# Performance work log

Hardware: AMD Instinct MI355X
Metric: run time of the kernel (lower is better)

## Reference

```python
import jax, jax.numpy as jnp
import numpy as np

B, T, I, Hd = 64, 1024, 256, 256
SIGMA = 0.01


def setup_inputs() -> dict:
    key = jax.random.key(0)
    ks = jax.random.split(key, 7)
    return {
        "inputs": jax.random.normal(ks[0], (B, T, I), dtype=jnp.float32),
        "W_xz": jax.random.normal(ks[1], (I, Hd), dtype=jnp.float32) * SIGMA,
        "W_hz": jax.random.normal(ks[2], (Hd, Hd), dtype=jnp.float32) * SIGMA,
        "b_z": jnp.zeros((Hd,), dtype=jnp.float32),
        "W_xr": jax.random.normal(ks[3], (I, Hd), dtype=jnp.float32) * SIGMA,
        "W_hr": jax.random.normal(ks[4], (Hd, Hd), dtype=jnp.float32) * SIGMA,
        "b_r": jnp.zeros((Hd,), dtype=jnp.float32),
        "W_xh": jax.random.normal(ks[5], (I, Hd), dtype=jnp.float32) * SIGMA,
        "W_hh": jax.random.normal(ks[6], (Hd, Hd), dtype=jnp.float32) * SIGMA,
        "b_h": jnp.zeros((Hd,), dtype=jnp.float32),
    }


def reference(inputs, W_xz, W_hz, b_z, W_xr, W_hr, b_r, W_xh, W_hh, b_h):
    # inputs: [B, T, I] -> time-major [T, B, I]
    xs = jnp.swapaxes(inputs, 0, 1)
    # Precompute all input-side projections in three big GEMMs (same math,
    # hoisted out of the recurrence): [T, B, Hd] each.
    xz = jnp.einsum("tbi,ih->tbh", xs, W_xz) + b_z
    xr = jnp.einsum("tbi,ih->tbh", xs, W_xr) + b_r
    xh = jnp.einsum("tbi,ih->tbh", xs, W_xh) + b_h

    H0 = jnp.zeros((inputs.shape[0], W_hz.shape[0]), dtype=inputs.dtype)

    def step(H, x):
        xz_t, xr_t, xh_t = x
        Z = jax.nn.sigmoid(xz_t + H @ W_hz)
        R = jax.nn.sigmoid(xr_t + H @ W_hr)
        H_tilde = jnp.tanh(xh_t + (R * H) @ W_hh)
        H_new = Z * H + (1.0 - Z) * H_tilde
        return H_new, H_new

    H_last, outs = jax.lax.scan(step, H0, (xz, xr, xh))
    # outputs stacked along dim=1: [B, T, Hd]
    outputs = jnp.swapaxes(outs, 0, 1)
    return outputs, H_last
```

## Files before the change

### kernel.cpp

```cpp
#include <hip/hip_runtime.h>
#include <math.h>

#define BB 64
#define TT 1024
#define II 256
#define HD 256

typedef unsigned short ushort_t;
typedef unsigned int uint_t;

typedef short sh8 __attribute__((ext_vector_type(8)));
typedef float fx4 __attribute__((ext_vector_type(4)));
typedef uint_t u32x4 __attribute__((ext_vector_type(4)));

__device__ __forceinline__ ushort_t f2bf(float f) {
    uint_t u = __float_as_uint(f);
    uint_t r = (u + 0x7fffu + ((u >> 16) & 1u)) >> 16;
    return (ushort_t)r;
}
__device__ __forceinline__ float bf2f(ushort_t v) {
    return __uint_as_float(((uint_t)v) << 16);
}

__device__ __forceinline__ float fast_rcp(float x) {
#if __has_builtin(__builtin_amdgcn_rcpf)
    return __builtin_amdgcn_rcpf(x);
#else
    return 1.f / x;
#endif
}
__device__ __forceinline__ float sigm(float x) {
    return fast_rcp(1.f + __expf(-x));
}
__device__ __forceinline__ float tanh_fast(float x) {
    return 1.f - 2.f * fast_rcp(1.f + __expf(2.f * x));
}

__device__ __forceinline__ fx4 mfma16(sh8 a, sh8 b, fx4 c) {
    return __builtin_amdgcn_mfma_f32_16x16x32_bf16(a, b, c, 0, 0, 0);
}

__device__ __forceinline__ void split2(float a, float b, uint_t& hi, uint_t& lo) {
    const uint_t ua = __float_as_uint(a), ub = __float_as_uint(b);
    hi = (ua >> 16) | (ub & 0xffff0000u);
    const float la = a - __uint_as_float(ua & 0xffff0000u);
    const float lb = b - __uint_as_float(ub & 0xffff0000u);
    const uint_t ula = __float_as_uint(la), ulb = __float_as_uint(lb);
    lo = (ula >> 16) | (ulb & 0xffff0000u);
}

__device__ __forceinline__ void async_g2l(const ushort_t* g, ushort_t* l) {
#if __has_builtin(__builtin_amdgcn_global_load_lds)
    __builtin_amdgcn_global_load_lds(
        (const __attribute__((address_space(1))) unsigned int*)g,
        (__attribute__((address_space(3))) unsigned int*)l, 16, 0, 0);
#else
    *reinterpret_cast<uint4*>(l) = *reinterpret_cast<const uint4*>(g);
#endif
}

#define BAR() asm volatile("s_waitcnt lgkmcnt(0)\n\ts_barrier" ::: "memory")

__global__ __launch_bounds__(256) void prepack_kernel(
    const float* __restrict__ Wz, const float* __restrict__ Wr,
    const float* __restrict__ Wh,
    const float* __restrict__ Xz, const float* __restrict__ Xr,
    const float* __restrict__ Xh,
    ushort_t* __restrict__ Tz, ushort_t* __restrict__ Tr,
    ushort_t* __restrict__ Th,
    ushort_t* __restrict__ Thi, ushort_t* __restrict__ Tlo)
{
    const int idx = blockIdx.x * 256 + threadIdx.x;
    const int j = idx >> 8;
    const int k = idx & 255;
    const int y = blockIdx.y;
    if (y < 3) {
        const float* W = (y == 0) ? Wz : (y == 1) ? Wr : Wh;
        ushort_t* T = (y == 0) ? Tz : (y == 1) ? Tr : Th;
        T[idx] = f2bf(W[k * HD + j]);
    } else {
        const int g = y - 3;
        const float* W = (g == 0) ? Xz : (g == 1) ? Xr : Xh;
        const float wv = W[k * HD + j];
        const ushort_t hi = f2bf(wv);
        Thi[g * 65536 + idx] = hi;
        Tlo[g * 65536 + idx] = f2bf(wv - bf2f(hi));
    }
}

__global__ __launch_bounds__(256) void proj_mfma(
    const float* __restrict__ X,
    const ushort_t* __restrict__ Thi, const ushort_t* __restrict__ Tlo,
    const float* __restrict__ bz, const float* __restrict__ br,
    const float* __restrict__ bh,
    ushort_t* __restrict__ x5)
{
    __shared__ __align__(16) ushort_t ep[64 * 256];

    const int tid  = threadIdx.x;
    const int lane = tid & 63;
    const int w    = tid >> 6;
    const int kq   = lane >> 4;
    const int ml   = lane & 15;
    const int m0   = blockIdx.x * 64;
    const int g    = blockIdx.y;

    const ushort_t* Bh = Thi + (size_t)g * 65536;
    const ushort_t* Bl = Tlo + (size_t)g * 65536;
    const float* bias = (g == 0) ? bz : (g == 1) ? br : bh;

    const fx4 zero4 = {0.f, 0.f, 0.f, 0.f};
    fx4 acc[4][4];
#pragma unroll
    for (int mt = 0; mt < 4; ++mt)
#pragma unroll
        for (int nt = 0; nt < 4; ++nt) acc[mt][nt] = zero4;

    for (int kt = 0; kt < 8; ++kt) {
        const int koff = kq * 8 + kt * 32;
        sh8 bhi[4], blo[4];
#pragma unroll
        for (int nt = 0; nt < 4; ++nt) {
            const size_t rb = (size_t)(w * 64 + nt * 16 + ml) * 256 + koff;
            bhi[nt] = *reinterpret_cast<const sh8*>(Bh + rb);
            blo[nt] = *reinterpret_cast<const sh8*>(Bl + rb);
        }
#pragma unroll
        for (int mt = 0; mt < 4; ++mt) {
            const float* xp = X + (size_t)(m0 + mt * 16 + ml) * II + koff;
            const float4 f0 = *reinterpret_cast<const float4*>(xp);
            const float4 f1 = *reinterpret_cast<const float4*>(xp + 4);
            uint_t hv0, hv1, hv2, hv3, lv0, lv1, lv2, lv3;
            split2(f0.x, f0.y, hv0, lv0);
            split2(f0.z, f0.w, hv1, lv1);
            split2(f1.x, f1.y, hv2, lv2);
            split2(f1.z, f1.w, hv3, lv3);
            const u32x4 hq = {hv0, hv1, hv2, hv3};
            const u32x4 lq = {lv0, lv1, lv2, lv3};
            const sh8 ahi = __builtin_bit_cast(sh8, hq);
            const sh8 alo = __builtin_bit_cast(sh8, lq);
#pragma unroll
            for (int nt = 0; nt < 4; ++nt) {
                acc[mt][nt] = mfma16(ahi, bhi[nt], acc[mt][nt]);
                acc[mt][nt] = mfma16(alo, bhi[nt], acc[mt][nt]);
                acc[mt][nt] = mfma16(ahi, blo[nt], acc[mt][nt]);
            }
        }
    }

#pragma unroll
    for (int nt = 0; nt < 4; ++nt) {
        const int col = w * 64 + nt * 16 + ml;
        const float bv = bias[col];
#pragma unroll
        for (int mt = 0; mt < 4; ++mt)
#pragma unroll
            for (int r = 0; r < 4; ++r)
                ep[(mt * 16 + kq * 4 + r) * 256 + col] =
                    f2bf(acc[mt][nt][r] + bv);
    }
    __syncthreads();

    const int b   = m0 >> 10;
    const int t0m = m0 & 1023;
    const uint4* eps = reinterpret_cast<const uint4*>(ep);
#pragma unroll
    for (int it = 0; it < 8; ++it) {
        const int idx  = it * 256 + tid;
        const int rr   = idx >> 5;
        const int part = idx & 31;
        uint4* dst = reinterpret_cast<uint4*>(
            x5 + ((size_t)(t0m + rr) * 64 + b) * 768 + g * 256) + part;
        *dst = eps[idx];
    }
}

#define XB_U16 768

__global__ __launch_bounds__(512, 1) void gru_recur(
    const ushort_t* __restrict__ x5,
    const ushort_t* __restrict__ Tz, const ushort_t* __restrict__ Tr,
    const ushort_t* __restrict__ Th,
    float* __restrict__ out)
{
    __shared__ __align__(16) ushort_t Hl[264];
    __shared__ __align__(16) ushort_t Rl[264];
    __shared__ __align__(16) ushort_t Xb[2][XB_U16];

    const int tid  = threadIdx.x;
    const int lane = tid & 63;
    const int w    = tid >> 6;
    const int kq   = lane >> 4;
    const int ml   = lane & 15;
    const int cl   = lane & 31;
    const int gate = lane >> 5;
    const int sel  = (lane >> 4) & 1;
    const int j    = w * 32 + cl;
    const int b    = blockIdx.x;

    sh8 wz[2][8], wr[2][8], wh[2][8];
#pragma unroll
    for (int cc = 0; cc < 2; ++cc) {
        const int jw = w * 32 + cc * 16 + ml;
        const size_t rb = (size_t)jw * 256 + kq * 8;
#pragma unroll
        for (int kt = 0; kt < 8; ++kt) {
            wz[cc][kt] = *reinterpret_cast<const sh8*>(Tz + rb + kt * 32);
            wr[cc][kt] = *reinterpret_cast<const sh8*>(Tr + rb + kt * 32);
            wh[cc][kt] = *reinterpret_cast<const sh8*>(Th + rb + kt * 32);
        }
    }

    if (tid < 132) { ((uint_t*)Hl)[tid] = 0u; ((uint_t*)Rl)[tid] = 0u; }

    float hk = 0.f;

    if (tid < 96) async_g2l(x5 + (size_t)b * XB_U16 + tid * 8, &Xb[0][tid * 8]);
    asm volatile("s_waitcnt vmcnt(0)" ::: "memory");
    __syncthreads();

    const ushort_t* harow = Hl + kq * 8;
    const ushort_t* rarow = Rl + kq * 8;
    float* ob = out + (size_t)b * TT * HD;

    const fx4 zero4 = {0.f, 0.f, 0.f, 0.f};
    int cur = 0;
    for (int t = 0; t < TT; ++t) {
        {
            const int tn = (t < TT - 1) ? t + 1 : t;
            if (tid < 96)
                async_g2l(x5 + ((size_t)tn * 64 + b) * XB_U16 + tid * 8,
                          &Xb[cur ^ 1][tid * 8]);
        }
        const ushort_t* xc = Xb[cur];

        const float hsh  = __shfl(hk, cl);
        const float xg   = bf2f(xc[gate * 256 + j]);
        const float xh_r = bf2f(xc[512 + j]);

        fx4 az0 = zero4, az1 = zero4, ar0 = zero4, ar1 = zero4;
#pragma unroll
        for (int kt = 0; kt < 8; ++kt) {
            const sh8 a = *reinterpret_cast<const sh8*>(harow + kt * 32);
            az0 = mfma16(a, wz[0][kt], az0);
            az1 = mfma16(a, wz[1][kt], az1);
            ar0 = mfma16(a, wr[0][kt], ar0);
            ar1 = mfma16(a, wr[1][kt], ar1);
        }
        const float v0 = gate ? ar0[0] : az0[0];
        const float v1 = gate ? ar1[0] : az1[0];
        const float v  = sel ? v1 : v0;
        const float s  = sigm(xg + v);
        const float zreg = s;
        if (gate) Rl[j] = f2bf(s * hsh);
        BAR();

        fx4 ah0a = zero4, ah0b = zero4, ah1a = zero4, ah1b = zero4;
#pragma unroll
        for (int kt = 0; kt < 8; kt += 2) {
            const sh8 a0 = *reinterpret_cast<const sh8*>(rarow + kt * 32);
            const sh8 a1 = *reinterpret_cast<const sh8*>(rarow + (kt + 1) * 32);
            ah0a = mfma16(a0, wh[0][kt], ah0a);
            ah1a = mfma16(a0, wh[1][kt], ah1a);
            ah0b = mfma16(a1, wh[0][kt + 1], ah0b);
            ah1b = mfma16(a1, wh[1][kt + 1], ah1b);
        }
        float hn = hk;
        if (!gate) {
            const float va = sel ? (ah1a[0] + ah1b[0]) : (ah0a[0] + ah0b[0]);
            const float th = tanh_fast(xh_r + va);
            hn = zreg * hk + (1.f - zreg) * th;
            hk = hn;
            Hl[j] = f2bf(hn);
        }
        asm volatile("s_waitcnt vmcnt(0)" ::: "memory");
        BAR();

        if (!gate) ob[(size_t)t * HD + j] = hn;
        cur ^= 1;
    }

    if (!gate) out[(size_t)BB * TT * HD + (size_t)b * HD + j] = hk;
}

extern "C" void kernel_launch(void* const* d_in, const int* in_sizes, int n_in,
                              void* d_out, int out_size, void* d_ws, size_t ws_size,
                              hipStream_t stream) {
    const float* X   = (const float*)d_in[0];
    const float* Wxz = (const float*)d_in[1];
    const float* Whz = (const float*)d_in[2];
    const float* bz  = (const float*)d_in[3];
    const float* Wxr = (const float*)d_in[4];
    const float* Whr = (const float*)d_in[5];
    const float* br  = (const float*)d_in[6];
    const float* Wxh = (const float*)d_in[7];
    const float* Whh = (const float*)d_in[8];
    const float* bh  = (const float*)d_in[9];
    float* out = (float*)d_out;

    const size_t X5_BYTES = (size_t)TT * BB * 3 * 256 * 2;
    ushort_t* x5  = (ushort_t*)d_ws;
    ushort_t* Tz  = (ushort_t*)((char*)d_ws + X5_BYTES);
    ushort_t* Tr  = Tz + HD * HD;
    ushort_t* Th  = Tr + HD * HD;
    ushort_t* Thi = Th + HD * HD;
    ushort_t* Tlo = Thi + 3 * HD * HD;

    prepack_kernel<<<dim3(256, 6), 256, 0, stream>>>(
        Whz, Whr, Whh, Wxz, Wxr, Wxh, Tz, Tr, Th, Thi, Tlo);
    proj_mfma<<<dim3(1024, 3), 256, 0, stream>>>(
        X, Thi, Tlo, bz, br, bh, x5);
    gru_recur<<<dim3(64), 512, 0, stream>>>(x5, Tz, Tr, Th, out);
}
```

Baseline: 1.412 ms.

## Split recurrent K-dimension between MFMA and VALU bf16 dot2 paths

The recurrent matvecs now run only the first half of K (128) through MFMA. The second half is computed on the vector ALU with bf16 dot2 instructions, using new pair-packed weight copies held in registers. The aim is to shorten the per-step MFMA dependency chain, which is latency-bound at batch 1 per block, by overlapping it with VALU work. In exchange it raises register use by 96 VGPRs per thread and adds LDS broadcast reads plus a cross-lane shuffle for the candidate gate.

After: 1.979 ms. 40.1% more time.

```diff
diff --git a/kernel.cpp b/kernel.cpp
--- a/kernel.cpp
+++ b/kernel.cpp
@@ -12,6 +12,7 @@
 typedef short sh8 __attribute__((ext_vector_type(8)));
 typedef float fx4 __attribute__((ext_vector_type(4)));
 typedef uint_t u32x4 __attribute__((ext_vector_type(4)));
+typedef __bf16 v2bf __attribute__((ext_vector_type(2)));
 
 __device__ __forceinline__ ushort_t f2bf(float f) {
     uint_t u = __float_as_uint(f);
@@ -20,6 +21,17 @@
 }
 __device__ __forceinline__ float bf2f(ushort_t v) {
     return __uint_as_float(((uint_t)v) << 16);
+}
+
+__device__ __forceinline__ float dot2bf(uint_t w, uint_t h, float acc) {
+#if __has_builtin(__builtin_amdgcn_fdot2_f32_bf16)
+    return __builtin_amdgcn_fdot2_f32_bf16(__builtin_bit_cast(v2bf, w),
+                                           __builtin_bit_cast(v2bf, h), acc, false);
+#else
+    acc += __uint_as_float(w << 16) * __uint_as_float(h << 16);
+    acc += __uint_as_float(w & 0xffff0000u) * __uint_as_float(h & 0xffff0000u);
+    return acc;
+#endif
 }
 
 __device__ __forceinline__ float fast_rcp(float x) {
@@ -68,19 +80,30 @@
     const float* __restrict__ Xh,
     ushort_t* __restrict__ Tz, ushort_t* __restrict__ Tr,
     ushort_t* __restrict__ Th,
+    uint_t* __restrict__ Pz, uint_t* __restrict__ Pr, uint_t* __restrict__ Ph,
     ushort_t* __restrict__ Thi, ushort_t* __restrict__ Tlo)
 {
     const int idx = blockIdx.x * 256 + threadIdx.x;
-    const int j = idx >> 8;
-    const int k = idx & 255;
     const int y = blockIdx.y;
     if (y < 3) {
         const float* W = (y == 0) ? Wz : (y == 1) ? Wr : Wh;
         ushort_t* T = (y == 0) ? Tz : (y == 1) ? Tr : Th;
+        uint_t* P = (y == 0) ? Pz : (y == 1) ? Pr : Ph;
+        const int j = idx >> 8;
+        const int k = idx & 255;
         T[idx] = f2bf(W[k * HD + j]);
+        if (idx < 32768) {
+            const int p = idx >> 8;
+            const int jj = idx & 255;
+            const ushort_t lo = f2bf(W[(2 * p) * HD + jj]);
+            const ushort_t hi = f2bf(W[(2 * p + 1) * HD + jj]);
+            P[idx] = ((uint_t)hi << 16) | lo;
+        }
     } else {
         const int g = y - 3;
         const float* W = (g == 0) ? Xz : (g == 1) ? Xr : Xh;
+        const int j = idx >> 8;
+        const int k = idx & 255;
         const float wv = W[k * HD + j];
         const ushort_t hi = f2bf(wv);
         Thi[g * 65536 + idx] = hi;
@@ -181,6 +204,8 @@
     const ushort_t* __restrict__ x5,
     const ushort_t* __restrict__ Tz, const ushort_t* __restrict__ Tr,
     const ushort_t* __restrict__ Th,
+    const uint_t* __restrict__ Pz, const uint_t* __restrict__ Pr,
+    const uint_t* __restrict__ Ph,
     float* __restrict__ out)
 {
     __shared__ __align__(16) ushort_t Hl[264];
@@ -198,17 +223,26 @@
     const int j    = w * 32 + cl;
     const int b    = blockIdx.x;
 
-    sh8 wz[2][8], wr[2][8], wh[2][8];
+    sh8 wz[2][4], wr[2][4], wh[2][4];
 #pragma unroll
     for (int cc = 0; cc < 2; ++cc) {
         const int jw = w * 32 + cc * 16 + ml;
         const size_t rb = (size_t)jw * 256 + kq * 8;
 #pragma unroll
-        for (int kt = 0; kt < 8; ++kt) {
+        for (int kt = 0; kt < 4; ++kt) {
             wz[cc][kt] = *reinterpret_cast<const sh8*>(Tz + rb + kt * 32);
             wr[cc][kt] = *reinterpret_cast<const sh8*>(Tr + rb + kt * 32);
             wh[cc][kt] = *reinterpret_cast<const sh8*>(Th + rb + kt * 32);
         }
+    }
+    uint_t vw1[64], vw2[32];
+    {
+        const uint_t* Pg = gate ? Pr : Pz;
+#pragma unroll
+        for (int i = 0; i < 64; ++i) vw1[i] = Pg[(size_t)(64 + i) * 256 + j];
+#pragma unroll
+        for (int i = 0; i < 32; ++i)
+            vw2[i] = Ph[(size_t)(64 + gate * 32 + i) * 256 + j];
     }
 
     if (tid < 132) { ((uint_t*)Hl)[tid] = 0u; ((uint_t*)Rl)[tid] = 0u; }
@@ -240,34 +274,52 @@
 
         fx4 az0 = zero4, az1 = zero4, ar0 = zero4, ar1 = zero4;
 #pragma unroll
-        for (int kt = 0; kt < 8; ++kt) {
+        for (int kt = 0; kt < 4; ++kt) {
             const sh8 a = *reinterpret_cast<const sh8*>(harow + kt * 32);
             az0 = mfma16(a, wz[0][kt], az0);
             az1 = mfma16(a, wz[1][kt], az1);
             ar0 = mfma16(a, wr[0][kt], ar0);
             ar1 = mfma16(a, wr[1][kt], ar1);
         }
+        float va0 = 0.f, va1 = 0.f, va2 = 0.f, va3 = 0.f;
+#pragma unroll
+        for (int u = 0; u < 16; ++u) {
+            const uint4 hv = *reinterpret_cast<const uint4*>(Hl + 128 + u * 8);
+            va0 = dot2bf(vw1[4 * u + 0], hv.x, va0);
+            va1 = dot2bf(vw1[4 * u + 1], hv.y, va1);
+            va2 = dot2bf(vw1[4 * u + 2], hv.z, va2);
+            va3 = dot2bf(vw1[4 * u + 3], hv.w, va3);
+        }
+        const float vval = (va0 + va1) + (va2 + va3);
         const float v0 = gate ? ar0[0] : az0[0];
         const float v1 = gate ? ar1[0] : az1[0];
-        const float v  = sel ? v1 : v0;
-        const float s  = sigm(xg + v);
+        const float s  = sigm(xg + (sel ? v1 : v0) + vval);
         const float zreg = s;
         if (gate) Rl[j] = f2bf(s * hsh);
         BAR();
 
-        fx4 ah0a = zero4, ah0b = zero4, ah1a = zero4, ah1b = zero4;
-#pragma unroll
-        for (int kt = 0; kt < 8; kt += 2) {
-            const sh8 a0 = *reinterpret_cast<const sh8*>(rarow + kt * 32);
-            const sh8 a1 = *reinterpret_cast<const sh8*>(rarow + (kt + 1) * 32);
-            ah0a = mfma16(a0, wh[0][kt], ah0a);
-            ah1a = mfma16(a0, wh[1][kt], ah1a);
-            ah0b = mfma16(a1, wh[0][kt + 1], ah0b);
-            ah1b = mfma16(a1, wh[1][kt + 1], ah1b);
-        }
+        fx4 ah0 = zero4, ah1 = zero4;
+#pragma unroll
+        for (int kt = 0; kt < 4; ++kt) {
+            const sh8 a = *reinterpret_cast<const sh8*>(rarow + kt * 32);
+            ah0 = mfma16(a, wh[0][kt], ah0);
+            ah1 = mfma16(a, wh[1][kt], ah1);
+        }
+        float vb0 = 0.f, vb1 = 0.f, vb2 = 0.f, vb3 = 0.f;
+#pragma unroll
+        for (int u = 0; u < 8; ++u) {
+            const uint4 rv = *reinterpret_cast<const uint4*>(
+                Rl + 128 + gate * 64 + u * 8);
+            vb0 = dot2bf(vw2[4 * u + 0], rv.x, vb0);
+            vb1 = dot2bf(vw2[4 * u + 1], rv.y, vb1);
+            vb2 = dot2bf(vw2[4 * u + 2], rv.z, vb2);
+            vb3 = dot2bf(vw2[4 * u + 3], rv.w, vb3);
+        }
+        float vh = (vb0 + vb1) + (vb2 + vb3);
+        vh += __shfl_xor(vh, 32);
         float hn = hk;
         if (!gate) {
-            const float va = sel ? (ah1a[0] + ah1b[0]) : (ah0a[0] + ah0b[0]);
+            const float va = (sel ? ah1[0] : ah0[0]) + vh;
             const float th = tanh_fast(xh_r + va);
             hn = zreg * hk + (1.f - zreg) * th;
             hk = hn;
@@ -305,10 +357,13 @@
     ushort_t* Th  = Tr + HD * HD;
     ushort_t* Thi = Th + HD * HD;
     ushort_t* Tlo = Thi + 3 * HD * HD;
+    uint_t*   Pz  = (uint_t*)(Tlo + 3 * HD * HD);
+    uint_t*   Pr  = Pz + 128 * HD;
+    uint_t*   Ph  = Pr + 128 * HD;
 
     prepack_kernel<<<dim3(256, 6), 256, 0, stream>>>(
-        Whz, Whr, Whh, Wxz, Wxr, Wxh, Tz, Tr, Th, Thi, Tlo);
+        Whz, Whr, Whh, Wxz, Wxr, Wxh, Tz, Tr, Th, Pz, Pr, Ph, Thi, Tlo);
     proj_mfma<<<dim3(1024, 3), 256, 0, stream>>>(
         X, Thi, Tlo, bz, br, bh, x5);
-    gru_recur<<<dim3(64), 512, 0, stream>>>(x5, Tz, Tr, Th, out);
-}
+    gru_recur<<<dim3(64), 512, 0, stream>>>(x5, Tz, Tr, Th, Pz, Pr, Ph, out);
+}
```

## Fuse three gate projections into one block with shared-memory X split

Applied to the files above, without the earlier changes.

The input projection kernel now computes all three gate projections (z, r, h) in one block over a 32-timestep tile of one batch row, instead of launching a separate grid slice per gate. X is loaded once, split into bf16 hi/lo halves, and staged in padded shared memory for reuse across the gates. This is meant to cut redundant global reads of X and repeated split conversions. In exchange it adds more shared memory, more accumulators per thread, and extra barriers in a per-gate epilogue.

After: 1.426 ms. Within noise of the previous version (+1.0%).

```diff
diff --git a/kernel.cpp b/kernel.cpp
--- a/kernel.cpp
+++ b/kernel.cpp
@@ -11,7 +11,6 @@
 
 typedef short sh8 __attribute__((ext_vector_type(8)));
 typedef float fx4 __attribute__((ext_vector_type(4)));
-typedef uint_t u32x4 __attribute__((ext_vector_type(4)));
 
 __device__ __forceinline__ ushort_t f2bf(float f) {
     uint_t u = __float_as_uint(f);
@@ -88,90 +87,108 @@
     }
 }
 
-__global__ __launch_bounds__(256) void proj_mfma(
+#define XROW 264
+
+__global__ __launch_bounds__(512) void proj_fused(
     const float* __restrict__ X,
     const ushort_t* __restrict__ Thi, const ushort_t* __restrict__ Tlo,
     const float* __restrict__ bz, const float* __restrict__ br,
     const float* __restrict__ bh,
     ushort_t* __restrict__ x5)
 {
-    __shared__ __align__(16) ushort_t ep[64 * 256];
+    __shared__ __align__(16) ushort_t Xs[2][32][XROW];
+    __shared__ __align__(16) ushort_t ep[32 * 256];
 
     const int tid  = threadIdx.x;
     const int lane = tid & 63;
     const int w    = tid >> 6;
     const int kq   = lane >> 4;
     const int ml   = lane & 15;
-    const int m0   = blockIdx.x * 64;
-    const int g    = blockIdx.y;
-
-    const ushort_t* Bh = Thi + (size_t)g * 65536;
-    const ushort_t* Bl = Tlo + (size_t)g * 65536;
-    const float* bias = (g == 0) ? bz : (g == 1) ? br : bh;
+    const int b    = blockIdx.x & 63;
+    const int tc   = blockIdx.x >> 6;
+    const int t0   = tc * 32;
+
+#pragma unroll
+    for (int i = 0; i < 4; ++i) {
+        const int idx = i * 512 + tid;
+        const int r   = idx >> 6;
+        const int c4  = idx & 63;
+        const float4 v = *reinterpret_cast<const float4*>(
+            X + (size_t)(b * 1024 + t0 + r) * II + c4 * 4);
+        uint_t h0, l0, h1, l1;
+        split2(v.x, v.y, h0, l0);
+        split2(v.z, v.w, h1, l1);
+        *reinterpret_cast<uint_t*>(&Xs[0][r][c4 * 4])     = h0;
+        *reinterpret_cast<uint_t*>(&Xs[0][r][c4 * 4 + 2]) = h1;
+        *reinterpret_cast<uint_t*>(&Xs[1][r][c4 * 4])     = l0;
+        *reinterpret_cast<uint_t*>(&Xs[1][r][c4 * 4 + 2]) = l1;
+    }
+    __syncthreads();
 
     const fx4 zero4 = {0.f, 0.f, 0.f, 0.f};
-    fx4 acc[4][4];
-#pragma unroll
-    for (int mt = 0; mt < 4; ++mt)
-#pragma unroll
-        for (int nt = 0; nt < 4; ++nt) acc[mt][nt] = zero4;
-
+    fx4 acc[3][2][2];
+#pragma unroll
+    for (int g = 0; g < 3; ++g)
+#pragma unroll
+        for (int mt = 0; mt < 2; ++mt)
+#pragma unroll
+            for (int nt = 0; nt < 2; ++nt) acc[g][mt][nt] = zero4;
+
+#pragma unroll
     for (int kt = 0; kt < 8; ++kt) {
         const int koff = kq * 8 + kt * 32;
-        sh8 bhi[4], blo[4];
-#pragma unroll
-        for (int nt = 0; nt < 4; ++nt) {
-            const size_t rb = (size_t)(w * 64 + nt * 16 + ml) * 256 + koff;
-            bhi[nt] = *reinterpret_cast<const sh8*>(Bh + rb);
-            blo[nt] = *reinterpret_cast<const sh8*>(Bl + rb);
-        }
-#pragma unroll
-        for (int mt = 0; mt < 4; ++mt) {
-            const float* xp = X + (size_t)(m0 + mt * 16 + ml) * II + koff;
-            const float4 f0 = *reinterpret_cast<const float4*>(xp);
-            const float4 f1 = *reinterpret_cast<const float4*>(xp + 4);
-            uint_t hv0, hv1, hv2, hv3, lv0, lv1, lv2, lv3;
-            split2(f0.x, f0.y, hv0, lv0);
-            split2(f0.z, f0.w, hv1, lv1);
-            split2(f1.x, f1.y, hv2, lv2);
-            split2(f1.z, f1.w, hv3, lv3);
-            const u32x4 hq = {hv0, hv1, hv2, hv3};
-            const u32x4 lq = {lv0, lv1, lv2, lv3};
-            const sh8 ahi = __builtin_bit_cast(sh8, hq);
-            const sh8 alo = __builtin_bit_cast(sh8, lq);
-#pragma unroll
-            for (int nt = 0; nt < 4; ++nt) {
-                acc[mt][nt] = mfma16(ahi, bhi[nt], acc[mt][nt]);
-                acc[mt][nt] = mfma16(alo, bhi[nt], acc[mt][nt]);
-                acc[mt][nt] = mfma16(ahi, blo[nt], acc[mt][nt]);
+        sh8 ahi[2], alo[2];
+#pragma unroll
+        for (int mt = 0; mt < 2; ++mt) {
+            ahi[mt] = *reinterpret_cast<const sh8*>(&Xs[0][mt * 16 + ml][koff]);
+            alo[mt] = *reinterpret_cast<const sh8*>(&Xs[1][mt * 16 + ml][koff]);
+        }
+#pragma unroll
+        for (int g = 0; g < 3; ++g) {
+            sh8 bhi[2], blo[2];
+#pragma unroll
+            for (int nt = 0; nt < 2; ++nt) {
+                const size_t rb = ((size_t)g << 16) +
+                    (size_t)(w * 32 + nt * 16 + ml) * 256 + koff;
+                bhi[nt] = *reinterpret_cast<const sh8*>(Thi + rb);
+                blo[nt] = *reinterpret_cast<const sh8*>(Tlo + rb);
             }
-        }
-    }
-
-#pragma unroll
-    for (int nt = 0; nt < 4; ++nt) {
-        const int col = w * 64 + nt * 16 + ml;
-        const float bv = bias[col];
-#pragma unroll
-        for (int mt = 0; mt < 4; ++mt)
-#pragma unroll
-            for (int r = 0; r < 4; ++r)
-                ep[(mt * 16 + kq * 4 + r) * 256 + col] =
-                    f2bf(acc[mt][nt][r] + bv);
-    }
-    __syncthreads();
-
-    const int b   = m0 >> 10;
-    const int t0m = m0 & 1023;
-    const uint4* eps = reinterpret_cast<const uint4*>(ep);
-#pragma unroll
-    for (int it = 0; it < 8; ++it) {
-        const int idx  = it * 256 + tid;
-        const int rr   = idx >> 5;
-        const int part = idx & 31;
-        uint4* dst = reinterpret_cast<uint4*>(
-            x5 + ((size_t)(t0m + rr) * 64 + b) * 768 + g * 256) + part;
-        *dst = eps[idx];
+#pragma unroll
+            for (int mt = 0; mt < 2; ++mt)
+#pragma unroll
+                for (int nt = 0; nt < 2; ++nt) {
+                    acc[g][mt][nt] = mfma16(ahi[mt], bhi[nt], acc[g][mt][nt]);
+                    acc[g][mt][nt] = mfma16(alo[mt], bhi[nt], acc[g][mt][nt]);
+                    acc[g][mt][nt] = mfma16(ahi[mt], blo[nt], acc[g][mt][nt]);
+                }
+        }
+    }
+
+    for (int g = 0; g < 3; ++g) {
+        const float* bias = (g == 0) ? bz : (g == 1) ? br : bh;
+        __syncthreads();
+#pragma unroll
+        for (int nt = 0; nt < 2; ++nt) {
+            const int col = w * 32 + nt * 16 + ml;
+            const float bv = bias[col];
+#pragma unroll
+            for (int mt = 0; mt < 2; ++mt)
+#pragma unroll
+                for (int r = 0; r < 4; ++r)
+                    ep[(mt * 16 + kq * 4 + r) * 256 + col] =
+                        f2bf(acc[g][mt][nt][r] + bv);
+        }
+        __syncthreads();
+        const uint4* eps = reinterpret_cast<const uint4*>(ep);
+#pragma unroll
+        for (int it = 0; it < 2; ++it) {
+            const int idx  = it * 512 + tid;
+            const int rr   = idx >> 5;
+            const int part = idx & 31;
+            uint4* dst = reinterpret_cast<uint4*>(
+                x5 + ((size_t)(t0 + rr) * 64 + b) * 768 + g * 256) + part;
+            *dst = eps[idx];
+        }
     }
 }
 
@@ -308,7 +325,7 @@
 
     prepack_kernel<<<dim3(256, 6), 256, 0, stream>>>(
         Whz, Whr, Whh, Wxz, Wxr, Wxh, Tz, Tr, Th, Thi, Tlo);
-    proj_mfma<<<dim3(1024, 3), 256, 0, stream>>>(
+    proj_fused<<<dim3(2048), 512, 0, stream>>>(
         X, Thi, Tlo, bz, br, bh, x5);
     gru_recur<<<dim3(64), 512, 0, stream>>>(x5, Tz, Tr, Th, out);
 }
```
